# Optimization experiments

Hardware: AMD Instinct MI355X
Metric: run time of the kernel (lower is better)

The kernel has to match this reference:

```python
import jax, jax.numpy as jnp
import numpy as np

N = 100_000   # total nodes per graph batch
E = 400_000   # directed edges per graph batch
G = 1024      # number of graphs
F_IN = 90


def _lin_init(key, fan_in, fan_out):
    s = 1.0 / np.sqrt(fan_in)
    kW, kb = jax.random.split(key)
    W = jax.random.uniform(kW, (fan_in, fan_out), jnp.float32, -s, s)
    b = jax.random.uniform(kb, (fan_out,), jnp.float32, -s, s)
    return W, b


def setup_inputs() -> dict:
    key = jax.random.key(0)
    ks = jax.random.split(key, 16)
    batch = (jnp.arange(N, dtype=jnp.int32) * G // N).astype(jnp.int32)
    inp = {
        'x1': jax.random.normal(ks[0], (N, F_IN), jnp.float32),
        'edge_index1': jax.random.randint(ks[1], (2, E), 0, N, jnp.int32),
        'batch1': batch,
        'x2': jax.random.normal(ks[2], (N, F_IN), jnp.float32),
        'edge_index2': jax.random.randint(ks[3], (2, E), 0, N, jnp.int32),
        'batch2': batch,
    }
    W1, b1 = _lin_init(ks[4], 90, 128)
    W2, b2 = _lin_init(ks[5], 128, 256)
    W3, b3 = _lin_init(ks[6], 256, 256)
    W4, b4 = _lin_init(ks[7], 256, 256)
    fc1_W, fc1_b = _lin_init(ks[8], 1024, 512)
    fc2_W, fc2_b = _lin_init(ks[9], 512, 256)
    fc3_W, fc3_b = _lin_init(ks[10], 256, 1)
    inp.update(W1=W1, b1=b1, W2=W2, b2=b2, W3=W3, b3=b3, W4=W4, b4=b4,
               fc1_W=fc1_W, fc1_b=fc1_b, fc2_W=fc2_W, fc2_b=fc2_b,
               fc3_W=fc3_W, fc3_b=fc3_b)
    return inp


def _gcn(x, W, b, src, dst, dinv):
    # GCNConv: D^{-1/2} (A + I) D^{-1/2} X W + b  (self-loops added)
    h = x @ W                                   # [N, F_out]
    norm = dinv[src] * dinv[dst]                # [E]
    agg = jax.ops.segment_sum(h[src] * norm[:, None], dst, num_segments=N)
    agg = agg + h * (dinv * dinv)[:, None]      # self-loop term
    return agg + b


def _drug_encoder(x, edge_index, batch, W1, b1, W2, b2, W3, b3, W4, b4):
    src, dst = edge_index[0], edge_index[1]
    # degree with self-loops (PyG gcn_norm)
    deg = jax.ops.segment_sum(jnp.ones(src.shape[0], x.dtype), dst, num_segments=N) + 1.0
    dinv = jax.lax.rsqrt(deg)
    x = jax.nn.relu(_gcn(x, W1, b1, src, dst, dinv))
    x = jax.nn.relu(_gcn(x, W2, b2, src, dst, dinv))
    x = jax.nn.relu(_gcn(x, W3, b3, src, dst, dinv))
    x = jax.nn.relu(_gcn(x, W4, b4, src, dst, dinv))
    gmax = jax.ops.segment_max(x, batch, num_segments=G)
    cnt = jax.ops.segment_sum(jnp.ones(N, x.dtype), batch, num_segments=G)
    gmean = jax.ops.segment_sum(x, batch, num_segments=G) / cnt[:, None]
    return jnp.concatenate([gmax, gmean], axis=1)   # [G, 512]


def reference(x1, edge_index1, batch1, x2, edge_index2, batch2,
              W1, b1, W2, b2, W3, b3, W4, b4,
              fc1_W, fc1_b, fc2_W, fc2_b, fc3_W, fc3_b):
    h1 = _drug_encoder(x1, edge_index1, batch1, W1, b1, W2, b2, W3, b3, W4, b4)
    h2 = _drug_encoder(x2, edge_index2, batch2, W1, b1, W2, b2, W3, b3, W4, b4)
    x = jnp.concatenate([h1 - h2, h2 - h1], axis=1)   # [G, 1024]
    x = jax.nn.relu(x @ fc1_W + fc1_b)                # dropout = identity (eval)
    x = jax.nn.relu(x @ fc2_W + fc2_b)
    x = jnp.tanh(x @ fc3_W + fc3_b)
    return x                                          # [G, 1]
```

## Files before the change

### kernel.cpp

```cpp
#include <hip/hip_runtime.h>
#include <hip/hip_bf16.h>

#define NN 100000
#define EE 400000
#define GG 1024

typedef _Float16 half_t;
typedef _Float16 f16x8 __attribute__((ext_vector_type(8)));
typedef float f32x4 __attribute__((ext_vector_type(4)));
typedef float f32x2 __attribute__((ext_vector_type(2)));

#define GLOAD_LDS(g, l) \
    __builtin_amdgcn_global_load_lds((const __attribute__((address_space(1))) void*)(g), \
                                     (__attribute__((address_space(3))) void*)(l), 16, 0, 0)


__global__ void k_count2(const int* __restrict__ ei1, const int* __restrict__ ei2,
                         int* __restrict__ deg) {
    int e = blockIdx.x * 256 + threadIdx.x;
    if (e >= 2 * EE) return;
    int enc = e >= EE;
    const int* ei = enc ? ei2 : ei1;
    int le = e - enc * EE;
    atomicAdd(&deg[enc * NN + ei[EE + le]], 1);
}

__global__ void k_scan_bsum(const int* __restrict__ deg, int* __restrict__ bsum, int total) {
    __shared__ int lds[256];
    int t = threadIdx.x;
    int base = blockIdx.x * 1024 + t * 4;
    int s = 0;
#pragma unroll
    for (int i = 0; i < 4; ++i) { int idx = base + i; s += (idx < total) ? deg[idx] : 0; }
    lds[t] = s;
    __syncthreads();
    for (int off = 128; off > 0; off >>= 1) {
        if (t < off) lds[t] += lds[t + off];
        __syncthreads();
    }
    if (t == 0) bsum[blockIdx.x] = lds[0];
}

__global__ void k_scan_write(const int* __restrict__ deg, const int* __restrict__ bsum,
                             int* __restrict__ rowptr, float* __restrict__ dinv,
                             int total, int totedge) {
    __shared__ int lds[256];
    __shared__ int blockoff;
    int t = threadIdx.x;
    if (t == 0) {
        int off = 0;
        for (int b = 0; b < (int)blockIdx.x; ++b) off += bsum[b];
        blockoff = off;
    }
    int base = blockIdx.x * 1024 + t * 4;
    int v[4]; int ts = 0;
#pragma unroll
    for (int i = 0; i < 4; ++i) { int idx = base + i; v[i] = (idx < total) ? deg[idx] : 0; ts += v[i]; }
    lds[t] = ts;
    __syncthreads();
    for (int off = 1; off < 256; off <<= 1) {
        int x = (t >= off) ? lds[t - off] : 0;
        __syncthreads();
        lds[t] += x;
        __syncthreads();
    }
    int excl = lds[t] - ts + blockoff;
#pragma unroll
    for (int i = 0; i < 4; ++i) {
        int idx = base + i;
        if (idx < total) {
            rowptr[idx] = excl;
            dinv[idx] = rsqrtf((float)v[i] + 1.0f);
        }
        excl += v[i];
    }
    if (blockIdx.x == 0 && t == 0) rowptr[total] = totedge;
}

__global__ void k_fill2(const int* __restrict__ ei1, const int* __restrict__ ei2,
                        const int* __restrict__ rowptr, int* __restrict__ cnt,
                        int* __restrict__ colv) {
    int e = blockIdx.x * 256 + threadIdx.x;
    if (e >= 2 * EE) return;
    int enc = e >= EE;
    const int* ei = enc ? ei2 : ei1;
    int le = e - enc * EE;
    int s = ei[le], d = ei[EE + le];
    int gd = enc * NN + d;
    int pos = rowptr[gd] + atomicAdd(&cnt[gd], 1);
    colv[pos] = s;
}

__global__ void k_starts2(const int* __restrict__ b1, const int* __restrict__ b2,
                          int* __restrict__ gstart) {
    int i = blockIdx.x * 256 + threadIdx.x;
    if (i >= 2 * NN) return;
    int enc = i >= NN;
    int il = i - enc * NN;
    const int* bat = enc ? b2 : b1;
    int* gs = gstart + enc * (GG + 1);
    int b = bat[il];
    if (il == 0) {
        for (int g = 0; g <= b; ++g) gs[g] = 0;
    } else {
        int pb = bat[il - 1];
        for (int g = pb + 1; g <= b; ++g) gs[g] = il;
    }
    if (il == NN - 1) {
        for (int g = b + 1; g <= GG; ++g) gs[g] = NN;
    }
}


__global__ void k_agg90(const float* __restrict__ x, const float* __restrict__ dinv,
                        const int* __restrict__ rowptr, const int* __restrict__ col,
                        half_t* __restrict__ out) {
    int wave = threadIdx.x >> 6;
    int lane = threadIdx.x & 63;
    int n = blockIdx.x * 4 + wave;
    if (n >= NN) return;
    bool al = lane < 45;
    float dn = dinv[n];
    f32x2 acc = {0.f, 0.f};
    if (al) acc = dn * ((const f32x2*)(x + (size_t)n * 90))[lane];
    int j0 = rowptr[n], j1 = rowptr[n + 1];
    int j = j0;
    for (; j + 4 <= j1; j += 4) {
        int s0 = col[j], s1 = col[j + 1], s2 = col[j + 2], s3 = col[j + 3];
        float d0 = dinv[s0], d1 = dinv[s1], d2 = dinv[s2], d3 = dinv[s3];
        if (al) {
            f32x2 v0 = ((const f32x2*)(x + (size_t)s0 * 90))[lane];
            f32x2 v1 = ((const f32x2*)(x + (size_t)s1 * 90))[lane];
            f32x2 v2 = ((const f32x2*)(x + (size_t)s2 * 90))[lane];
            f32x2 v3 = ((const f32x2*)(x + (size_t)s3 * 90))[lane];
            acc += d0 * v0; acc += d1 * v1; acc += d2 * v2; acc += d3 * v3;
        }
    }
    for (; j < j1; ++j) {
        int s = col[j];
        float ds = dinv[s];
        if (al) acc += ds * ((const f32x2*)(x + (size_t)s * 90))[lane];
    }
    float v0 = al ? dn * acc[0] : 0.f;
    float v1 = al ? dn * acc[1] : 0.f;
    half_t h0 = (half_t)v0, l0 = (half_t)(v0 - (float)h0);
    half_t h1 = (half_t)v1, l1 = (half_t)(v1 - (float)h1);
    half_t* o = out + (size_t)n * 256;
    o[2 * lane] = h0;
    o[2 * lane + 1] = h1;
    o[128 + 2 * lane] = l0;
    o[128 + 2 * lane + 1] = l1;
}

template <int VW>
__global__ void k_aggpair(const float* __restrict__ x, const float* __restrict__ dinv,
                          const int* __restrict__ rowptr, const int* __restrict__ col,
                          half_t* __restrict__ out) {
    constexpr int F = 32 * VW;
    typedef float fvec __attribute__((ext_vector_type(VW)));
    int wave = threadIdx.x >> 6;
    int lane = threadIdx.x & 63;
    int sub = lane & 31;
    int n = blockIdx.x * 8 + wave * 2 + (lane >> 5);
    float dn = dinv[n];
    fvec acc = dn * ((const fvec*)(x + (size_t)n * F))[sub];
    int j0 = rowptr[n];
    int deg = rowptr[n + 1] - j0;
    int m = max(deg, __shfl_xor(deg, 32));
    int t = 0;
    for (; t + 4 <= m; t += 4) {
        bool o0 = t < deg, o1 = t + 1 < deg, o2 = t + 2 < deg, o3 = t + 3 < deg;
        int s0 = o0 ? col[j0 + t]     : n;
        int s1 = o1 ? col[j0 + t + 1] : n;
        int s2 = o2 ? col[j0 + t + 2] : n;
        int s3 = o3 ? col[j0 + t + 3] : n;
        float w0 = o0 ? dinv[s0] : 0.f;
        float w1 = o1 ? dinv[s1] : 0.f;
        float w2 = o2 ? dinv[s2] : 0.f;
        float w3 = o3 ? dinv[s3] : 0.f;
        fvec v0 = ((const fvec*)(x + (size_t)s0 * F))[sub];
        fvec v1 = ((const fvec*)(x + (size_t)s1 * F))[sub];
        fvec v2 = ((const fvec*)(x + (size_t)s2 * F))[sub];
        fvec v3 = ((const fvec*)(x + (size_t)s3 * F))[sub];
        acc += w0 * v0; acc += w1 * v1; acc += w2 * v2; acc += w3 * v3;
    }
    if (t < m) {
        bool o0 = t < deg, o1 = t + 1 < deg, o2 = t + 2 < deg;
        bool m1 = t + 1 < m, m2 = t + 2 < m;
        int s0 = o0 ? col[j0 + t]     : n;
        int s1 = o1 ? col[j0 + t + 1] : n;
        int s2 = o2 ? col[j0 + t + 2] : n;
        float w0 = o0 ? dinv[s0] : 0.f;
        float w1 = o1 ? dinv[s1] : 0.f;
        float w2 = o2 ? dinv[s2] : 0.f;
        fvec v0 = ((const fvec*)(x + (size_t)s0 * F))[sub];
        acc += w0 * v0;
        if (m1) { fvec v1 = ((const fvec*)(x + (size_t)s1 * F))[sub]; acc += w1 * v1; }
        if (m2) { fvec v2 = ((const fvec*)(x + (size_t)s2 * F))[sub]; acc += w2 * v2; }
    }
    half_t* o = out + (size_t)n * (2 * F);
#pragma unroll
    for (int i = 0; i < VW; ++i) {
        float v = dn * acc[i];
        half_t h = (half_t)v;
        half_t l = (half_t)(v - (float)h);
        o[sub * VW + i] = h;
        o[F + sub * VW + i] = l;
    }
}


__global__ void k_wprep(const float* __restrict__ W, half_t* __restrict__ Bt,
                        int K, int Kpad, int Nc) {
    int t = blockIdx.x * 256 + threadIdx.x;
    if (t >= Nc * Kpad) return;
    int n = t / Kpad, kp = t % Kpad;
    half_t h = (half_t)0.f, l = (half_t)0.f;
    if (kp < K) {
        float w = W[(size_t)kp * Nc + n];
        h = (half_t)w;
        l = (half_t)(w - (float)h);
    }
    half_t* o = Bt + (size_t)n * 3 * Kpad;
    o[kp] = h;
    o[Kpad + kp] = h;
    o[2 * Kpad + kp] = l;
}

__global__ void k_split(const float* __restrict__ in, half_t* __restrict__ out, int K) {
    int t = blockIdx.x * 256 + threadIdx.x;
    int row = t / K, k = t % K;
    float v = in[t];
    half_t h = (half_t)v;
    half_t l = (half_t)(v - (float)h);
    half_t* o = out + (size_t)row * 2 * K;
    o[k] = h;
    o[K + k] = l;
}


template <bool RELU>
__global__ __launch_bounds__(256, 2)
void k_mgemm(const half_t* __restrict__ Ap, const half_t* __restrict__ Bt,
             const float* __restrict__ bias, float* __restrict__ C,
             int M, int Kpad, int Nc) {
    __shared__ half_t As[128 * 64];
    __shared__ half_t Bs[128 * 64];
    const int tid = threadIdx.x;
    const int wave = tid >> 6, lane = tid & 63;
    const int wm = wave >> 1, wn = wave & 1;
    const int bm = blockIdx.x * 128, bn = blockIdx.y * 128;
    const int KA = 2 * Kpad, KB = 3 * Kpad;
    const int nkt = KB >> 6;
    const int aTiles = KA >> 6;

    f32x4 acc[4][4] = {};

    const int srow = tid >> 3;
    const int ch = tid & 7;

    for (int kt = 0; kt < nkt; ++kt) {
        int ka0 = ((kt < aTiles) ? kt : (kt - aTiles)) << 6;
        int kb0 = kt << 6;
        __syncthreads();
#pragma unroll
        for (int i = 0; i < 4; ++i) {
            int rl = i * 32 + srow;
            int sch = ch ^ (rl & 7);
            int gr = bm + rl; if (gr >= M) gr = M - 1;
            const half_t* ga = Ap + (size_t)gr * KA + ka0 + sch * 8;
            GLOAD_LDS(ga, (char*)As + i * 4096 + wave * 1024);
        }
#pragma unroll
        for (int i = 0; i < 4; ++i) {
            int rl = i * 32 + srow;
            int sch = ch ^ (rl & 7);
            const half_t* gb = Bt + (size_t)(bn + rl) * KB + kb0 + sch * 8;
            GLOAD_LDS(gb, (char*)Bs + i * 4096 + wave * 1024);
        }
        __syncthreads();
#pragma unroll
        for (int s = 0; s < 2; ++s) {
            f16x8 af[4], bf[4];
#pragma unroll
            for (int i = 0; i < 4; ++i) {
                int row = wm * 64 + i * 16 + (lane & 15);
                int c = s * 4 + (lane >> 4);
                af[i] = *(const f16x8*)&As[row * 64 + ((c ^ (row & 7)) << 3)];
            }
#pragma unroll
            for (int j = 0; j < 4; ++j) {
                int row = wn * 64 + j * 16 + (lane & 15);
                int c = s * 4 + (lane >> 4);
                bf[j] = *(const f16x8*)&Bs[row * 64 + ((c ^ (row & 7)) << 3)];
            }
#pragma unroll
            for (int i = 0; i < 4; ++i)
#pragma unroll
                for (int j = 0; j < 4; ++j)
                    acc[i][j] = __builtin_amdgcn_mfma_f32_16x16x32_f16(af[i], bf[j], acc[i][j], 0, 0, 0);
        }
    }

#pragma unroll
    for (int i = 0; i < 4; ++i) {
#pragma unroll
        for (int j = 0; j < 4; ++j) {
            int cc = bn + wn * 64 + j * 16 + (lane & 15);
            float bv = bias[cc];
            int r0 = bm + wm * 64 + i * 16 + (lane >> 4) * 4;
#pragma unroll
            for (int q = 0; q < 4; ++q) {
                int gr = r0 + q;
                if (gr < M) {
                    float v = acc[i][j][q] + bv;
                    if (RELU) v = fmaxf(v, 0.f);
                    C[(size_t)gr * Nc + cc] = v;
                }
            }
        }
    }
}


template <bool RELU>
__global__ __launch_bounds__(256, 2)
void k_mgemm256(const half_t* __restrict__ Ap, const half_t* __restrict__ Bt,
                const float* __restrict__ bias, float* __restrict__ C,
                int M, int Kpad) {
    __shared__ half_t As[128 * 64];
    __shared__ half_t Bs[256 * 64];
    const int tid = threadIdx.x;
    const int wave = tid >> 6, lane = tid & 63;
    const int wm = wave >> 1, wn = wave & 1;
    const int bm = blockIdx.x * 128;
    const int KA = 2 * Kpad, KB = 3 * Kpad;
    const int nkt = KB >> 6;
    const int aTiles = KA >> 6;

    f32x4 acc[4][8] = {};

    const int srow = tid >> 3;
    const int ch = tid & 7;

    for (int kt = 0; kt < nkt; ++kt) {
        int ka0 = ((kt < aTiles) ? kt : (kt - aTiles)) << 6;
        int kb0 = kt << 6;
        __syncthreads();
#pragma unroll
        for (int i = 0; i < 4; ++i) {
            int rl = i * 32 + srow;
            int sch = ch ^ (rl & 7);
            int gr = bm + rl; if (gr >= M) gr = M - 1;
            const half_t* ga = Ap + (size_t)gr * KA + ka0 + sch * 8;
            GLOAD_LDS(ga, (char*)As + i * 4096 + wave * 1024);
        }
#pragma unroll
        for (int i = 0; i < 8; ++i) {
            int rl = i * 32 + srow;
            int sch = ch ^ (rl & 7);
            const half_t* gb = Bt + (size_t)rl * KB + kb0 + sch * 8;
            GLOAD_LDS(gb, (char*)Bs + i * 4096 + wave * 1024);
        }
        __syncthreads();
#pragma unroll
        for (int s = 0; s < 2; ++s) {
            f16x8 af[4], bf[8];
#pragma unroll
            for (int i = 0; i < 4; ++i) {
                int row = wm * 64 + i * 16 + (lane & 15);
                int c = s * 4 + (lane >> 4);
                af[i] = *(const f16x8*)&As[row * 64 + ((c ^ (row & 7)) << 3)];
            }
#pragma unroll
            for (int j = 0; j < 8; ++j) {
                int row = wn * 128 + j * 16 + (lane & 15);
                int c = s * 4 + (lane >> 4);
                bf[j] = *(const f16x8*)&Bs[row * 64 + ((c ^ (row & 7)) << 3)];
            }
#pragma unroll
            for (int i = 0; i < 4; ++i)
#pragma unroll
                for (int j = 0; j < 8; ++j)
                    acc[i][j] = __builtin_amdgcn_mfma_f32_16x16x32_f16(af[i], bf[j], acc[i][j], 0, 0, 0);
        }
    }

#pragma unroll
    for (int i = 0; i < 4; ++i) {
#pragma unroll
        for (int j = 0; j < 8; ++j) {
            int cc = wn * 128 + j * 16 + (lane & 15);
            float bv = bias[cc];
            int r0 = bm + wm * 64 + i * 16 + (lane >> 4) * 4;
#pragma unroll
            for (int q = 0; q < 4; ++q) {
                int gr = r0 + q;
                if (gr < M) {
                    float v = acc[i][j][q] + bv;
                    if (RELU) v = fmaxf(v, 0.f);
                    C[(size_t)gr * 256 + cc] = v;
                }
            }
        }
    }
}


__global__ void k_pool(const float* __restrict__ act, const int* __restrict__ gstart,
                       float* __restrict__ h) {
    int g = blockIdx.x;
    int f = threadIdx.x;
    int s = gstart[g], e = gstart[g + 1];
    float mx = 0.f, sm = 0.f;
    for (int i = s; i < e; ++i) {
        float v = act[(size_t)i * 256 + f];
        mx = fmaxf(mx, v);
        sm += v;
    }
    float cnt = (float)(e - s);
    h[(size_t)g * 512 + f] = mx;
    h[(size_t)g * 512 + 256 + f] = (cnt > 0.f) ? sm / cnt : 0.f;
}


__global__ void k_headin_split(const float* __restrict__ h, half_t* __restrict__ xh) {
    int t = blockIdx.x * blockDim.x + threadIdx.x;
    if (t >= GG * 1024) return;
    int g = t >> 10, j = t & 1023;
    const float* h1 = h + (size_t)g * 512;
    const float* h2 = h + (size_t)(GG + g) * 512;
    float v = (j < 512) ? (h1[j] - h2[j]) : (h2[j - 512] - h1[j - 512]);
    half_t hi = (half_t)v;
    half_t lo = (half_t)(v - (float)hi);
    half_t* o = xh + (size_t)g * 2048;
    o[j] = hi;
    o[1024 + j] = lo;
}

__global__ void k_fc3(const float* __restrict__ A, const float* __restrict__ W,
                      const float* __restrict__ b, float* __restrict__ out) {
    int g = blockIdx.x * 4 + (threadIdx.x >> 6);
    int lane = threadIdx.x & 63;
    const float* a = A + (size_t)g * 256;
    float p = a[lane] * W[lane] + a[lane + 64] * W[lane + 64]
            + a[lane + 128] * W[lane + 128] + a[lane + 192] * W[lane + 192];
    for (int off = 32; off > 0; off >>= 1) p += __shfl_down(p, off);
    if (lane == 0) out[g] = tanhf(p + b[0]);
}


extern "C" void kernel_launch(void* const* d_in, const int* in_sizes, int n_in,
                              void* d_out, int out_size, void* d_ws, size_t ws_size,
                              hipStream_t stream) {
    const float* x1  = (const float*)d_in[0];
    const int*   ei1 = (const int*)d_in[1];
    const int*   ba1 = (const int*)d_in[2];
    const float* x2  = (const float*)d_in[3];
    const int*   ei2 = (const int*)d_in[4];
    const int*   ba2 = (const int*)d_in[5];
    const float* W1 = (const float*)d_in[6];
    const float* b1 = (const float*)d_in[7];
    const float* W2 = (const float*)d_in[8];
    const float* b2 = (const float*)d_in[9];
    const float* W3 = (const float*)d_in[10];
    const float* b3 = (const float*)d_in[11];
    const float* W4 = (const float*)d_in[12];
    const float* b4 = (const float*)d_in[13];
    const float* fc1W = (const float*)d_in[14];
    const float* fc1b = (const float*)d_in[15];
    const float* fc2W = (const float*)d_in[16];
    const float* fc2b = (const float*)d_in[17];
    const float* fc3W = (const float*)d_in[18];
    const float* fc3b = (const float*)d_in[19];
    float* out = (float*)d_out;

    char* ws = (char*)d_ws;
    size_t off = 0;
    auto alloc = [&](size_t bytes) -> void* {
        void* p = (void*)(ws + off);
        off += (bytes + 255) & ~(size_t)255;
        return p;
    };
    int*    dc     = (int*)alloc((size_t)4 * NN * sizeof(int));
    int*    rowptr = (int*)alloc((size_t)(2 * NN + 1) * sizeof(int));
    int*    colv   = (int*)alloc((size_t)2 * EE * sizeof(int));
    int*    bsum   = (int*)alloc(256 * sizeof(int));
    int*    gstart = (int*)alloc((size_t)2 * (GG + 1) * sizeof(int));
    float*  dinv   = (float*)alloc((size_t)2 * NN * sizeof(float));
    half_t* Ap     = (half_t*)alloc((size_t)NN * 512 * sizeof(half_t));
    float*  act    = (float*)alloc((size_t)NN * 256 * sizeof(float));
    half_t* Bt1    = (half_t*)alloc((size_t)128 * 384 * sizeof(half_t));
    half_t* Bt2    = (half_t*)alloc((size_t)256 * 384 * sizeof(half_t));
    half_t* Bt3    = (half_t*)alloc((size_t)256 * 768 * sizeof(half_t));
    half_t* Bt4    = (half_t*)alloc((size_t)256 * 768 * sizeof(half_t));
    half_t* Btf1   = (half_t*)alloc((size_t)512 * 3072 * sizeof(half_t));
    half_t* Btf2   = (half_t*)alloc((size_t)256 * 1536 * sizeof(half_t));
    float*  hpool  = (float*)alloc((size_t)2 * GG * 512 * sizeof(float));
    half_t* xhs    = (half_t*)alloc((size_t)GG * 2048 * sizeof(half_t));
    float*  t1     = (float*)alloc((size_t)GG * 512 * sizeof(float));
    half_t* t1s    = (half_t*)alloc((size_t)GG * 1024 * sizeof(half_t));
    float*  t2     = (float*)alloc((size_t)GG * 256 * sizeof(float));

    int* deg = dc;
    int* cnt = dc + 2 * NN;

    int nsb2 = (2 * NN + 1023) / 1024;
    int mt = (NN + 127) / 128;

    k_wprep<<<(128 * 128 + 255) / 256, 256, 0, stream>>>(W1, Bt1, 90, 128, 128);
    k_wprep<<<(256 * 128 + 255) / 256, 256, 0, stream>>>(W2, Bt2, 128, 128, 256);
    k_wprep<<<(256 * 256 + 255) / 256, 256, 0, stream>>>(W3, Bt3, 256, 256, 256);
    k_wprep<<<(256 * 256 + 255) / 256, 256, 0, stream>>>(W4, Bt4, 256, 256, 256);
    k_wprep<<<(512 * 1024 + 255) / 256, 256, 0, stream>>>(fc1W, Btf1, 1024, 1024, 512);
    k_wprep<<<(256 * 512 + 255) / 256, 256, 0, stream>>>(fc2W, Btf2, 512, 512, 256);

    hipMemsetAsync(dc, 0, (size_t)4 * NN * sizeof(int), stream);
    k_count2<<<(2 * EE + 255) / 256, 256, 0, stream>>>(ei1, ei2, deg);
    k_scan_bsum<<<nsb2, 256, 0, stream>>>(deg, bsum, 2 * NN);
    k_scan_write<<<nsb2, 256, 0, stream>>>(deg, bsum, rowptr, dinv, 2 * NN, 2 * EE);
    k_fill2<<<(2 * EE + 255) / 256, 256, 0, stream>>>(ei1, ei2, rowptr, cnt, colv);
    k_starts2<<<(2 * NN + 255) / 256, 256, 0, stream>>>(ba1, ba2, gstart);

    for (int p = 0; p < 2; ++p) {
        const float* x  = p ? x2 : x1;
        const int*   rp = rowptr + p * NN;
        const float* dv = dinv + p * NN;
        const int*   gs = gstart + p * (GG + 1);

        k_agg90<<<(NN + 3) / 4, 256, 0, stream>>>(x, dv, rp, colv, Ap);
        k_mgemm<true><<<dim3(mt, 1), 256, 0, stream>>>(Ap, Bt1, b1, act, NN, 128, 128);
        k_aggpair<4><<<NN / 8, 256, 0, stream>>>(act, dv, rp, colv, Ap);
        k_mgemm256<true><<<mt, 256, 0, stream>>>(Ap, Bt2, b2, act, NN, 128);
        k_aggpair<8><<<NN / 8, 256, 0, stream>>>(act, dv, rp, colv, Ap);
        k_mgemm256<true><<<mt, 256, 0, stream>>>(Ap, Bt3, b3, act, NN, 256);
        k_aggpair<8><<<NN / 8, 256, 0, stream>>>(act, dv, rp, colv, Ap);
        k_mgemm256<true><<<mt, 256, 0, stream>>>(Ap, Bt4, b4, act, NN, 256);

        k_pool<<<GG, 256, 0, stream>>>(act, gs, hpool + (size_t)p * GG * 512);
    }

    k_headin_split<<<(GG * 1024 + 255) / 256, 256, 0, stream>>>(hpool, xhs);
    k_mgemm<true><<<dim3(GG / 128, 4), 256, 0, stream>>>(xhs, Btf1, fc1b, t1, GG, 1024, 512);
    k_split<<<(GG * 512 + 255) / 256, 256, 0, stream>>>(t1, t1s, 512);
    k_mgemm<true><<<dim3(GG / 128, 2), 256, 0, stream>>>(t1s, Btf2, fc2b, t2, GG, 512, 256);
    k_fc3<<<GG / 4, 256, 0, stream>>>(t2, fc3W, fc3b, out);
}
```

Before: 1.376 ms.

## Aggregate one node per wave, merge weight prep, parallelize block offset scan

The sparse aggregation kernels now give each full 64-lane wave a single node with narrower per-lane vectors (2 or 4 floats) instead of packing two nodes per wave with wider vectors. This removes the divergent max-degree loop shared across half-waves and keeps lanes doing useful work. The six weight-prep launches are merged into one kernel, and the serial per-block prefix over block sums in the scan is replaced by a single-block parallel scan kernel. The trade-off is narrower per-lane loads and one extra small launch.

```diff
diff --git a/kernel.cpp b/kernel.cpp
--- a/kernel.cpp
+++ b/kernel.cpp
@@ -41,17 +41,27 @@
     if (t == 0) bsum[blockIdx.x] = lds[0];
 }
 
-__global__ void k_scan_write(const int* __restrict__ deg, const int* __restrict__ bsum,
+__global__ void k_scan_off(const int* __restrict__ bsum, int* __restrict__ boff, int nb) {
+    __shared__ int lds[256];
+    int t = threadIdx.x;
+    int v = (t < nb) ? bsum[t] : 0;
+    lds[t] = v;
+    __syncthreads();
+    for (int off = 1; off < 256; off <<= 1) {
+        int x = (t >= off) ? lds[t - off] : 0;
+        __syncthreads();
+        lds[t] += x;
+        __syncthreads();
+    }
+    if (t < nb) boff[t] = lds[t] - v;
+}
+
+__global__ void k_scan_write(const int* __restrict__ deg, const int* __restrict__ boff,
                              int* __restrict__ rowptr, float* __restrict__ dinv,
                              int total, int totedge) {
     __shared__ int lds[256];
-    __shared__ int blockoff;
     int t = threadIdx.x;
-    if (t == 0) {
-        int off = 0;
-        for (int b = 0; b < (int)blockIdx.x; ++b) off += bsum[b];
-        blockoff = off;
-    }
+    int blockoff = boff[blockIdx.x];
     int base = blockIdx.x * 1024 + t * 4;
     int v[4]; int ts = 0;
 #pragma unroll
@@ -153,67 +163,49 @@
 }
 
 template <int VW>
-__global__ void k_aggpair(const float* __restrict__ x, const float* __restrict__ dinv,
-                          const int* __restrict__ rowptr, const int* __restrict__ col,
-                          half_t* __restrict__ out) {
-    constexpr int F = 32 * VW;
+__global__ void k_agg_splitv(const float* __restrict__ x, const float* __restrict__ dinv,
+                             const int* __restrict__ rowptr, const int* __restrict__ col,
+                             half_t* __restrict__ out) {
+    constexpr int F = 64 * VW;
     typedef float fvec __attribute__((ext_vector_type(VW)));
     int wave = threadIdx.x >> 6;
     int lane = threadIdx.x & 63;
-    int sub = lane & 31;
-    int n = blockIdx.x * 8 + wave * 2 + (lane >> 5);
+    int n = blockIdx.x * 4 + wave;
+    if (n >= NN) return;
     float dn = dinv[n];
-    fvec acc = dn * ((const fvec*)(x + (size_t)n * F))[sub];
-    int j0 = rowptr[n];
-    int deg = rowptr[n + 1] - j0;
-    int m = max(deg, __shfl_xor(deg, 32));
-    int t = 0;
-    for (; t + 4 <= m; t += 4) {
-        bool o0 = t < deg, o1 = t + 1 < deg, o2 = t + 2 < deg, o3 = t + 3 < deg;
-        int s0 = o0 ? col[j0 + t]     : n;
-        int s1 = o1 ? col[j0 + t + 1] : n;
-        int s2 = o2 ? col[j0 + t + 2] : n;
-        int s3 = o3 ? col[j0 + t + 3] : n;
-        float w0 = o0 ? dinv[s0] : 0.f;
-        float w1 = o1 ? dinv[s1] : 0.f;
-        float w2 = o2 ? dinv[s2] : 0.f;
-        float w3 = o3 ? dinv[s3] : 0.f;
-        fvec v0 = ((const fvec*)(x + (size_t)s0 * F))[sub];
-        fvec v1 = ((const fvec*)(x + (size_t)s1 * F))[sub];
-        fvec v2 = ((const fvec*)(x + (size_t)s2 * F))[sub];
-        fvec v3 = ((const fvec*)(x + (size_t)s3 * F))[sub];
-        acc += w0 * v0; acc += w1 * v1; acc += w2 * v2; acc += w3 * v3;
-    }
-    if (t < m) {
-        bool o0 = t < deg, o1 = t + 1 < deg, o2 = t + 2 < deg;
-        bool m1 = t + 1 < m, m2 = t + 2 < m;
-        int s0 = o0 ? col[j0 + t]     : n;
-        int s1 = o1 ? col[j0 + t + 1] : n;
-        int s2 = o2 ? col[j0 + t + 2] : n;
-        float w0 = o0 ? dinv[s0] : 0.f;
-        float w1 = o1 ? dinv[s1] : 0.f;
-        float w2 = o2 ? dinv[s2] : 0.f;
-        fvec v0 = ((const fvec*)(x + (size_t)s0 * F))[sub];
-        acc += w0 * v0;
-        if (m1) { fvec v1 = ((const fvec*)(x + (size_t)s1 * F))[sub]; acc += w1 * v1; }
-        if (m2) { fvec v2 = ((const fvec*)(x + (size_t)s2 * F))[sub]; acc += w2 * v2; }
+    fvec acc = dn * ((const fvec*)(x + (size_t)n * F))[lane];
+    int j0 = rowptr[n], j1 = rowptr[n + 1];
+    int j = j0;
+    for (; j + 4 <= j1; j += 4) {
+        int s0 = col[j], s1 = col[j + 1], s2 = col[j + 2], s3 = col[j + 3];
+        float d0 = dinv[s0], d1 = dinv[s1], d2 = dinv[s2], d3 = dinv[s3];
+        fvec v0 = ((const fvec*)(x + (size_t)s0 * F))[lane];
+        fvec v1 = ((const fvec*)(x + (size_t)s1 * F))[lane];
+        fvec v2 = ((const fvec*)(x + (size_t)s2 * F))[lane];
+        fvec v3 = ((const fvec*)(x + (size_t)s3 * F))[lane];
+        acc += d0 * v0; acc += d1 * v1; acc += d2 * v2; acc += d3 * v3;
+    }
+    for (; j < j1; ++j) {
+        int s = col[j];
+        acc += dinv[s] * ((const fvec*)(x + (size_t)s * F))[lane];
     }
     half_t* o = out + (size_t)n * (2 * F);
+    half_t hv[VW], lv[VW];
 #pragma unroll
     for (int i = 0; i < VW; ++i) {
         float v = dn * acc[i];
-        half_t h = (half_t)v;
-        half_t l = (half_t)(v - (float)h);
-        o[sub * VW + i] = h;
-        o[F + sub * VW + i] = l;
-    }
-}
-
-
-__global__ void k_wprep(const float* __restrict__ W, half_t* __restrict__ Bt,
-                        int K, int Kpad, int Nc) {
-    int t = blockIdx.x * 256 + threadIdx.x;
-    if (t >= Nc * Kpad) return;
+        hv[i] = (half_t)v;
+        lv[i] = (half_t)(v - (float)hv[i]);
+    }
+#pragma unroll
+    for (int i = 0; i < VW; ++i) o[lane * VW + i] = hv[i];
+#pragma unroll
+    for (int i = 0; i < VW; ++i) o[F + lane * VW + i] = lv[i];
+}
+
+
+__device__ __forceinline__ void wprep_one(const float* __restrict__ W, half_t* __restrict__ Bt,
+                                          int K, int Kpad, int Nc, int t) {
     int n = t / Kpad, kp = t % Kpad;
     half_t h = (half_t)0.f, l = (half_t)0.f;
     if (kp < K) {
@@ -225,6 +217,26 @@
     o[kp] = h;
     o[Kpad + kp] = h;
     o[2 * Kpad + kp] = l;
+}
+
+__global__ void k_wprep_all(const float* __restrict__ W1, const float* __restrict__ W2,
+                            const float* __restrict__ W3, const float* __restrict__ W4,
+                            const float* __restrict__ F1, const float* __restrict__ F2,
+                            half_t* __restrict__ B1, half_t* __restrict__ B2,
+                            half_t* __restrict__ B3, half_t* __restrict__ B4,
+                            half_t* __restrict__ Bf1, half_t* __restrict__ Bf2) {
+    int t = blockIdx.x * 256 + threadIdx.x;
+    if (t < 16384) { wprep_one(W1, B1, 90, 128, 128, t); return; }
+    t -= 16384;
+    if (t < 32768) { wprep_one(W2, B2, 128, 128, 256, t); return; }
+    t -= 32768;
+    if (t < 65536) { wprep_one(W3, B3, 256, 256, 256, t); return; }
+    t -= 65536;
+    if (t < 65536) { wprep_one(W4, B4, 256, 256, 256, t); return; }
+    t -= 65536;
+    if (t < 524288) { wprep_one(F1, Bf1, 1024, 1024, 512, t); return; }
+    t -= 524288;
+    if (t < 131072) { wprep_one(F2, Bf2, 512, 512, 256, t); return; }
 }
 
 __global__ void k_split(const float* __restrict__ in, half_t* __restrict__ out, int K) {
@@ -486,6 +498,7 @@
     int*    rowptr = (int*)alloc((size_t)(2 * NN + 1) * sizeof(int));
     int*    colv   = (int*)alloc((size_t)2 * EE * sizeof(int));
     int*    bsum   = (int*)alloc(256 * sizeof(int));
+    int*    boff   = (int*)alloc(256 * sizeof(int));
     int*    gstart = (int*)alloc((size_t)2 * (GG + 1) * sizeof(int));
     float*  dinv   = (float*)alloc((size_t)2 * NN * sizeof(float));
     half_t* Ap     = (half_t*)alloc((size_t)NN * 512 * sizeof(half_t));
@@ -508,17 +521,14 @@
     int nsb2 = (2 * NN + 1023) / 1024;
     int mt = (NN + 127) / 128;
 
-    k_wprep<<<(128 * 128 + 255) / 256, 256, 0, stream>>>(W1, Bt1, 90, 128, 128);
-    k_wprep<<<(256 * 128 + 255) / 256, 256, 0, stream>>>(W2, Bt2, 128, 128, 256);
-    k_wprep<<<(256 * 256 + 255) / 256, 256, 0, stream>>>(W3, Bt3, 256, 256, 256);
-    k_wprep<<<(256 * 256 + 255) / 256, 256, 0, stream>>>(W4, Bt4, 256, 256, 256);
-    k_wprep<<<(512 * 1024 + 255) / 256, 256, 0, stream>>>(fc1W, Btf1, 1024, 1024, 512);
-    k_wprep<<<(256 * 512 + 255) / 256, 256, 0, stream>>>(fc2W, Btf2, 512, 512, 256);
+    k_wprep_all<<<(835584 + 255) / 256, 256, 0, stream>>>(W1, W2, W3, W4, fc1W, fc2W,
+                                                          Bt1, Bt2, Bt3, Bt4, Btf1, Btf2);
 
     hipMemsetAsync(dc, 0, (size_t)4 * NN * sizeof(int), stream);
     k_count2<<<(2 * EE + 255) / 256, 256, 0, stream>>>(ei1, ei2, deg);
     k_scan_bsum<<<nsb2, 256, 0, stream>>>(deg, bsum, 2 * NN);
-    k_scan_write<<<nsb2, 256, 0, stream>>>(deg, bsum, rowptr, dinv, 2 * NN, 2 * EE);
+    k_scan_off<<<1, 256, 0, stream>>>(bsum, boff, nsb2);
+    k_scan_write<<<nsb2, 256, 0, stream>>>(deg, boff, rowptr, dinv, 2 * NN, 2 * EE);
     k_fill2<<<(2 * EE + 255) / 256, 256, 0, stream>>>(ei1, ei2, rowptr, cnt, colv);
     k_starts2<<<(2 * NN + 255) / 256, 256, 0, stream>>>(ba1, ba2, gstart);
 
@@ -530,11 +540,11 @@
 
         k_agg90<<<(NN + 3) / 4, 256, 0, stream>>>(x, dv, rp, colv, Ap);
         k_mgemm<true><<<dim3(mt, 1), 256, 0, stream>>>(Ap, Bt1, b1, act, NN, 128, 128);
-        k_aggpair<4><<<NN / 8, 256, 0, stream>>>(act, dv, rp, colv, Ap);
+        k_agg_splitv<2><<<(NN + 3) / 4, 256, 0, stream>>>(act, dv, rp, colv, Ap);
         k_mgemm256<true><<<mt, 256, 0, stream>>>(Ap, Bt2, b2, act, NN, 128);
-        k_aggpair<8><<<NN / 8, 256, 0, stream>>>(act, dv, rp, colv, Ap);
+        k_agg_splitv<4><<<(NN + 3) / 4, 256, 0, stream>>>(act, dv, rp, colv, Ap);
         k_mgemm256<true><<<mt, 256, 0, stream>>>(Ap, Bt3, b3, act, NN, 256);
-        k_aggpair<8><<<NN / 8, 256, 0, stream>>>(act, dv, rp, colv, Ap);
+        k_agg_splitv<4><<<(NN + 3) / 4, 256, 0, stream>>>(act, dv, rp, colv, Ap);
         k_mgemm256<true><<<mt, 256, 0, stream>>>(Ap, Bt4, b4, act, NN, 256);
 
         k_pool<<<GG, 256, 0, stream>>>(act, gs, hpool + (size_t)p * GG * 512);
```

Measured after the change: 1.331 ms. 3.2% less time.
